# Kernel tuning notes

Hardware: AMD Instinct MI355X
Metric: run time of the kernel (lower is better)

## Reference

```python
import jax, jax.numpy as jnp
import numpy as np
from jax import lax

D_MODEL = 1024
D_INNER = 2048
B = 8
T = 2048
INIT_ALPHA_BIAS = 2.0


def setup_inputs() -> dict:
    key = jax.random.key(0)
    ks = jax.random.split(key, 6)
    def xavier(k, shape):
        fan_in, fan_out = shape[1], shape[0]
        lim = float(np.sqrt(6.0 / (fan_in + fan_out)))
        return jax.random.uniform(k, shape, jnp.float32, -lim, lim)
    return {
        "x": jax.random.normal(ks[0], (B, T, D_MODEL), jnp.float32),
        "h0": jnp.zeros((B, D_INNER), jnp.float32),
        "W_in": xavier(ks[1], (D_INNER, D_MODEL)),
        "W_alpha": xavier(ks[2], (D_INNER, D_INNER)),
        "b_alpha": jnp.full((D_INNER,), INIT_ALPHA_BIAS, jnp.float32),
        "W_v": xavier(ks[3], (D_INNER, D_INNER)),
        "b_v": jnp.zeros((D_INNER,), jnp.float32),
        "W_out": xavier(ks[4], (D_MODEL, D_INNER)),
    }


def reference(x, h0, W_in, W_alpha, b_alpha, W_v, b_v, W_out):
    # in_proj + silu pre-activation: [B,T,D_inner]
    x_proj = jax.nn.silu(jnp.einsum('btd,id->bti', x, W_in))
    # time-major for the scan: [T,B,D_inner]
    xr = jnp.transpose(x_proj, (1, 0, 2))
    # precompute gate and value for all steps (big GEMMs)
    alpha = jax.nn.sigmoid(jnp.einsum('tbd,ed->tbe', xr, W_alpha) + b_alpha)
    v = jnp.einsum('tbd,ed->tbe', xr, W_v) + b_v

    def step(h, av):
        a, vt = av
        h_new = a * h + (1.0 - a) * vt  # decay-gated update
        out_t = h_new * jax.nn.silu(h_new)  # self-gating
        return h_new, out_t

    h_final, outs = lax.scan(step, h0, (alpha, v))  # outs: [T,B,D_inner]
    # out_proj back to model dim, batch-major: [B,T,D_model]
    output = jnp.einsum('tbe,de->btd', outs, W_out)
    return output, h_final
```

## Files before the change

kernel.cpp:

```cpp
#include <hip/hip_runtime.h>
#include <cstdint>
#include <cstddef>

typedef unsigned short u16;
typedef unsigned int   u32;

#define D_MODEL 1024
#define D_INNER 2048
#define BATCH   8
#define TSEQ    2048
#define MROWS   (BATCH*TSEQ)
#define CHUNK   32
#define NCHUNK  (TSEQ/CHUNK)
#define EDIM    (BATCH*D_INNER)

typedef float  f32x4  __attribute__((ext_vector_type(4)));
typedef __bf16 bf16x8 __attribute__((ext_vector_type(8)));
typedef short  s16x8  __attribute__((ext_vector_type(8)));

__device__ __forceinline__ float bf2f(u16 u){ return __builtin_bit_cast(float, (u32)u << 16); }
__device__ __forceinline__ u16 f2bf(float f){
  u32 u = __builtin_bit_cast(u32, f);
  u += 0x7fffu + ((u >> 16) & 1u);
  return (u16)(u >> 16);
}
__device__ __forceinline__ float sigm(float x){ return 1.0f/(1.0f + __expf(-x)); }

__device__ __forceinline__ void gld16(const u16* g, u16* l){
  __builtin_amdgcn_global_load_lds((const __attribute__((address_space(1))) void*)g,
                                   (__attribute__((address_space(3))) void*)l, 16, 0, 0);
}

__device__ __forceinline__ s16x8 cvt8(const float* s){
  float4 u0 = *(const float4*)s;
  float4 u1 = *(const float4*)(s + 4);
  s16x8 p;
  p[0]=(short)f2bf(u0.x); p[1]=(short)f2bf(u0.y);
  p[2]=(short)f2bf(u0.z); p[3]=(short)f2bf(u0.w);
  p[4]=(short)f2bf(u1.x); p[5]=(short)f2bf(u1.y);
  p[6]=(short)f2bf(u1.z); p[7]=(short)f2bf(u1.w);
  return p;
}

template<int MODE, int K, int N>
__global__ __launch_bounds__(512, 2) void gemm256(
    const u16* __restrict__ A, const u16* __restrict__ Bt,
    const float* __restrict__ bias, void* __restrict__ Cout)
{
  __shared__ __align__(16) u16 sAB[2][2][16384];
  constexpr int NT = K/64;
  const int tid = threadIdx.x;
  const int w = tid >> 6, lane = tid & 63;
  const int wr = w >> 2, wc = w & 3;
  const int l15 = lane & 15, kg = lane >> 4;
  const int bm = blockIdx.x, bn = blockIdx.y;

  const int st_row8 = w*8 + (lane>>3);
  const int st_colb = ((lane&7)*16) ^ (((lane>>5)&1)<<5);
  const size_t a_base = (size_t)(bm*256) * K + (st_colb>>1);
  const size_t b_base = (size_t)(bn*256) * K + (st_colb>>1);

  auto stageA = [&](int buf, int kt, int upper){
    u16* dst = &sAB[0][buf][upper*8192 + w*512];
    #pragma unroll
    for (int i = 0; i < 2; ++i){
      int row = upper*128 + i*64 + st_row8;
      gld16(A + a_base + (size_t)row*K + kt*64, dst + i*4096);
    }
  };
  auto stageB = [&](int buf, int kt, int upper){
    u16* dst = &sAB[1][buf][upper*8192 + w*512];
    #pragma unroll
    for (int i = 0; i < 2; ++i){
      int row = upper*128 + i*64 + st_row8;
      gld16(Bt + b_base + (size_t)row*K + kt*64, dst + i*4096);
    }
  };

  const int sw   = ((l15>>2)&1)<<5;
  const int rdA0 = ((wr*128 + l15)*128 + kg*16) ^ sw;
  const int rdB0 = ((wc*64  + l15)*128 + kg*16) ^ sw;

  f32x4 acc[8][4] = {};

  stageA(0, 0, 0); stageB(0, 0, 0); stageA(0, 0, 1); stageB(0, 0, 1);
  asm volatile("s_waitcnt vmcnt(4)" ::: "memory");
  __builtin_amdgcn_s_barrier();

  for (int t = 0; t < NT; ++t){
    const char* As = (const char*)&sAB[0][t&1][0];
    const char* Bs = (const char*)&sAB[1][t&1][0];
    const int nb = (t+1)&1;
    const bool more = (t < NT-1);
    #pragma unroll
    for (int q = 0; q < 4; ++q){
      const int mh = (q>>1) ^ (q&1);
      const int nh = q>>1;
      s16x8 af[4][2], bf[2][2];
      #pragma unroll
      for (int mf = 0; mf < 4; ++mf)
        #pragma unroll
        for (int ks = 0; ks < 2; ++ks)
          af[mf][ks] = *(const s16x8*)(As + rdA0 + mh*8192 + mf*2048 + ks*64);
      #pragma unroll
      for (int nf = 0; nf < 2; ++nf)
        #pragma unroll
        for (int ks = 0; ks < 2; ++ks)
          bf[nf][ks] = *(const s16x8*)(Bs + rdB0 + nh*4096 + nf*2048 + ks*64);
      if (more){
        if      (q == 0) stageA(nb, t+1, 0);
        else if (q == 1) stageB(nb, t+1, 0);
        else if (q == 2) stageA(nb, t+1, 1);
        else             stageB(nb, t+1, 1);
        asm volatile("s_waitcnt vmcnt(4)" ::: "memory");
      } else {
        asm volatile("s_waitcnt vmcnt(0)" ::: "memory");
      }
      __builtin_amdgcn_s_barrier();
      __builtin_amdgcn_s_setprio(1);
      #pragma unroll
      for (int mf = 0; mf < 4; ++mf)
        #pragma unroll
        for (int nf = 0; nf < 2; ++nf)
          #pragma unroll
          for (int ks = 0; ks < 2; ++ks)
            acc[mh*4+mf][nh*2+nf] = __builtin_amdgcn_mfma_f32_16x16x32_bf16(
                __builtin_bit_cast(bf16x8, af[mf][ks]),
                __builtin_bit_cast(bf16x8, bf[nf][ks]),
                acc[mh*4+mf][nh*2+nf], 0, 0, 0);
      __builtin_amdgcn_s_setprio(0);
      __builtin_amdgcn_s_barrier();
    }
  }

  #pragma unroll
  for (int mi = 0; mi < 8; ++mi){
    #pragma unroll
    for (int ni = 0; ni < 4; ++ni){
      #pragma unroll
      for (int r = 0; r < 4; ++r){
        const int row = bm*256 + wr*128 + mi*16 + kg*4 + r;
        const int col = bn*256 + wc*64 + ni*16 + l15;
        float val = acc[mi][ni][r];
        if constexpr (MODE == 0){
          val = val * sigm(val);
          ((u16*)Cout)[(size_t)row*N + col] = f2bf(val);
        } else if constexpr (MODE == 1){
          val = sigm(val + bias[col]);
          ((u16*)Cout)[(size_t)row*N + col] = f2bf(val);
        } else if constexpr (MODE == 2){
          val = val + bias[col];
          ((u16*)Cout)[(size_t)row*N + col] = f2bf(val);
        } else {
          const int orow = (row & 7)*TSEQ + (row >> 3);
          ((float*)Cout)[(size_t)orow*N + col] = val;
        }
      }
    }
  }
}

template<int MODE, int K, int N, bool BA, bool BB>
__global__ __launch_bounds__(256) void gemm_bt(
    const void* __restrict__ Ap, const void* __restrict__ Bp,
    const float* __restrict__ bias, void* __restrict__ Cout)
{
  __shared__ __align__(16) u16 sA[128*32];
  __shared__ __align__(16) u16 sB[128*32];
  const int tid = threadIdx.x;
  const int bm = blockIdx.x, bn = blockIdx.y;
  const int w = tid >> 6, lane = tid & 63;
  const int wr = w >> 1, wc = w & 1;
  const int l15 = lane & 15, kg = lane >> 4;
  const int r0   = tid >> 2;
  const int koff = (tid & 3) * 8;

  int ga[2];
  #pragma unroll
  for (int i = 0; i < 2; ++i){
    int mc = bm*128 + r0 + i*64;
    if (MODE == 0)      ga[i] = (mc & 7) * TSEQ + (mc >> 3);
    else if (MODE == 3) ga[i] = (mc & (TSEQ-1)) * BATCH + (mc >> 11);
    else                ga[i] = mc;
  }
  const u16*   Abf = (const u16*)Ap;
  const float* Af  = (const float*)Ap;
  const u16*   Bbf = (const u16*)Bp;
  const float* Bf  = (const float*)Bp;
  u16* la[2] = { sA + w*512, sA + 2048 + w*512 };
  u16* lb[2] = { sB + w*512, sB + 2048 + w*512 };
  u16* ldsA = sA + tid*8;
  u16* ldsB = sB + tid*8;
  const int gb[2] = { bn*128 + r0, bn*128 + r0 + 64 };

  f32x4 acc[4][4] = {};
  for (int kt = 0; kt < K/32; ++kt){
    __syncthreads();
    if constexpr (BA){
      gld16(Abf + (size_t)ga[0]*K + koff + kt*32, la[0]);
      gld16(Abf + (size_t)ga[1]*K + koff + kt*32, la[1]);
    } else {
      #pragma unroll
      for (int i = 0; i < 2; ++i)
        *(s16x8*)(ldsA + i*2048) = cvt8(Af + (size_t)ga[i]*K + koff + kt*32);
    }
    if constexpr (BB){
      gld16(Bbf + (size_t)gb[0]*K + koff + kt*32, lb[0]);
      gld16(Bbf + (size_t)gb[1]*K + koff + kt*32, lb[1]);
    } else {
      #pragma unroll
      for (int i = 0; i < 2; ++i)
        *(s16x8*)(ldsB + i*2048) = cvt8(Bf + (size_t)gb[i]*K + koff + kt*32);
    }
    __syncthreads();

    s16x8 af[4], bfr[4];
    #pragma unroll
    for (int m = 0; m < 4; ++m)
      af[m] = *(const s16x8*)(sA + (wr*64 + m*16 + l15)*32 + kg*8);
    #pragma unroll
    for (int n = 0; n < 4; ++n)
      bfr[n] = *(const s16x8*)(sB + (wc*64 + n*16 + l15)*32 + kg*8);
    #pragma unroll
    for (int m = 0; m < 4; ++m)
      #pragma unroll
      for (int n = 0; n < 4; ++n)
        acc[m][n] = __builtin_amdgcn_mfma_f32_16x16x32_bf16(
            __builtin_bit_cast(bf16x8, af[m]),
            __builtin_bit_cast(bf16x8, bfr[n]),
            acc[m][n], 0, 0, 0);
  }
  #pragma unroll
  for (int m = 0; m < 4; ++m)
    #pragma unroll
    for (int n = 0; n < 4; ++n)
      #pragma unroll
      for (int r = 0; r < 4; ++r){
        const int row = bm*128 + wr*64 + m*16 + kg*4 + r;
        const int col = bn*128 + wc*64 + n*16 + l15;
        float val = acc[m][n][r];
        if constexpr (MODE == 0){
          val = val * sigm(val);
          ((u16*)Cout)[(size_t)row*N + col] = f2bf(val);
        } else if constexpr (MODE == 1){
          val = sigm(val + bias[col]);
          ((u16*)Cout)[(size_t)row*N + col] = f2bf(val);
        } else if constexpr (MODE == 2){
          val = val + bias[col];
          ((u16*)Cout)[(size_t)row*N + col] = f2bf(val);
        } else {
          ((float*)Cout)[(size_t)row*N + col] = val;
        }
      }
}

__global__ __launch_bounds__(256) void scan_pass1(
    const u16* __restrict__ alpha, const u16* __restrict__ v,
    float* __restrict__ P, float* __restrict__ H)
{
  const int e = blockIdx.x*256 + threadIdx.x;
  const int c = blockIdx.y;
  const size_t base = (size_t)c*CHUNK*EDIM + e;
  float p = 1.f, h = 0.f;
  #pragma unroll 8
  for (int t = 0; t < CHUNK; ++t){
    float a  = bf2f(alpha[base + (size_t)t*EDIM]);
    float vv = bf2f(v[base + (size_t)t*EDIM]);
    p *= a;
    h = a*h + (1.f - a)*vv;
  }
  P[(size_t)c*EDIM + e] = p;
  H[(size_t)c*EDIM + e] = h;
}

__global__ __launch_bounds__(256) void scan_pass2(
    const float* __restrict__ P, const float* __restrict__ H,
    const float* __restrict__ h0, float* __restrict__ hstart,
    float* __restrict__ hfinal)
{
  const int e = blockIdx.x*256 + threadIdx.x;
  float hs = h0[e];
  for (int c = 0; c < NCHUNK; ++c){
    hstart[(size_t)c*EDIM + e] = hs;
    hs = P[(size_t)c*EDIM + e]*hs + H[(size_t)c*EDIM + e];
  }
  hfinal[e] = hs;
}

__global__ __launch_bounds__(256) void scan_pass3(
    const u16* __restrict__ alpha, const u16* __restrict__ v,
    const float* __restrict__ hstart, u16* __restrict__ outs)
{
  const int e = blockIdx.x*256 + threadIdx.x;
  const int c = blockIdx.y;
  const size_t base = (size_t)c*CHUNK*EDIM + e;
  float h = hstart[(size_t)c*EDIM + e];
  #pragma unroll 8
  for (int t = 0; t < CHUNK; ++t){
    float a  = bf2f(alpha[base + (size_t)t*EDIM]);
    float vv = bf2f(v[base + (size_t)t*EDIM]);
    h = a*h + (1.f - a)*vv;
    float o = h*h*sigm(h);
    outs[base + (size_t)t*EDIM] = f2bf(o);
  }
}

__global__ __launch_bounds__(256) void cvt_bf16(
    const float* __restrict__ src, u16* __restrict__ dst, int n4)
{
  const int i = blockIdx.x*256 + threadIdx.x;
  if (i >= n4) return;
  const float4 f = ((const float4*)src)[i];
  u32 w0 = (u32)f2bf(f.x) | ((u32)f2bf(f.y) << 16);
  u32 w1 = (u32)f2bf(f.z) | ((u32)f2bf(f.w) << 16);
  ((uint2*)dst)[i] = make_uint2(w0, w1);
}

__global__ __launch_bounds__(256) void cvt_x_tm(
    const float* __restrict__ src, u16* __restrict__ dst)
{
  const int i = blockIdx.x*256 + threadIdx.x;
  const int d4  = i & 255;
  const int rin = i >> 8;
  const int b = rin >> 11, tt = rin & (TSEQ-1);
  const int rout = tt*BATCH + b;
  const float4 f = ((const float4*)src)[i];
  u32 w0 = (u32)f2bf(f.x) | ((u32)f2bf(f.y) << 16);
  u32 w1 = (u32)f2bf(f.z) | ((u32)f2bf(f.w) << 16);
  ((uint2*)dst)[(size_t)rout*256 + d4] = make_uint2(w0, w1);
}

extern "C" void kernel_launch(void* const* d_in, const int* in_sizes, int n_in,
                              void* d_out, int out_size, void* d_ws, size_t ws_size,
                              hipStream_t stream)
{
  const float* x     = (const float*)d_in[0];
  const float* h0    = (const float*)d_in[1];
  const float* W_in  = (const float*)d_in[2];
  const float* W_al  = (const float*)d_in[3];
  const float* b_al  = (const float*)d_in[4];
  const float* W_v   = (const float*)d_in[5];
  const float* b_v   = (const float*)d_in[6];
  const float* W_out = (const float*)d_in[7];

  float* out  = (float*)d_out;
  float* hfin = out + (size_t)MROWS*D_MODEL;

  const size_t SZ_ACT = (size_t)MROWS*D_INNER*2;
  const size_t SZ_ST  = (size_t)NCHUNK*EDIM*4;
  const size_t SZ_WI  = (size_t)D_INNER*D_MODEL*2;
  const size_t SZ_WA  = (size_t)D_INNER*D_INNER*2;
  const size_t need_min  = 3*SZ_ACT + 3*SZ_ST;
  const size_t need_fast = need_min + 2*SZ_WI + 2*SZ_WA + 8192;

  if (ws_size < need_min) return;

  char* ws = (char*)d_ws;
  auto carve = [&](size_t bytes){
    char* p = ws; ws += (bytes + 255) & ~(size_t)255; return p;
  };
  u16* xp   = (u16*)carve(SZ_ACT);
  u16* alp  = (u16*)carve(SZ_ACT);
  u16* vv   = (u16*)carve(SZ_ACT);
  float* P  = (float*)carve(SZ_ST);
  float* H  = (float*)carve(SZ_ST);
  float* hs = (float*)carve(SZ_ST);

  const dim3 gScan(EDIM/256, NCHUNK);

  auto cvt = [&](const float* s, u16* d, size_t n){
    int n4 = (int)(n/4);
    cvt_bf16<<<(n4+255)/256, 256, 0, stream>>>(s, d, n4);
  };

  if (ws_size >= need_fast){
    u16* wib = (u16*)carve(SZ_WI);
    u16* wab = (u16*)carve(SZ_WA);
    u16* wvb = (u16*)carve(SZ_WA);
    u16* wob = (u16*)carve(SZ_WI);
    u16* xb  = alp;

    cvt_x_tm<<<(MROWS*D_MODEL/4)/256, 256, 0, stream>>>(x, xb);
    cvt(W_in,  wib, (size_t)D_INNER*D_MODEL);
    cvt(W_al,  wab, (size_t)D_INNER*D_INNER);
    cvt(W_v,   wvb, (size_t)D_INNER*D_INNER);
    cvt(W_out, wob, (size_t)D_MODEL*D_INNER);

    gemm256<0, D_MODEL, D_INNER><<<dim3(MROWS/256, D_INNER/256), 512, 0, stream>>>(xb, wib, nullptr, xp);
    gemm256<1, D_INNER, D_INNER><<<dim3(MROWS/256, D_INNER/256), 512, 0, stream>>>(xp, wab, b_al,    alp);
    gemm256<2, D_INNER, D_INNER><<<dim3(MROWS/256, D_INNER/256), 512, 0, stream>>>(xp, wvb, b_v,     vv);

    scan_pass1<<<gScan, 256, 0, stream>>>(alp, vv, P, H);
    scan_pass2<<<EDIM/256, 256, 0, stream>>>(P, H, h0, hs, hfin);
    scan_pass3<<<gScan, 256, 0, stream>>>(alp, vv, hs, vv);

    gemm256<3, D_INNER, D_MODEL><<<dim3(MROWS/256, D_MODEL/256), 512, 0, stream>>>(vv, wob, nullptr, out);
  } else {
    const dim3 gBig(MROWS/128, D_INNER/128);
    const dim3 gOut(MROWS/128, D_MODEL/128);
    gemm_bt<0, D_MODEL, D_INNER, false, false><<<gBig, 256, 0, stream>>>(x,  W_in, nullptr, xp);
    gemm_bt<1, D_INNER, D_INNER, true,  false><<<gBig, 256, 0, stream>>>(xp, W_al, b_al,    alp);
    gemm_bt<2, D_INNER, D_INNER, true,  false><<<gBig, 256, 0, stream>>>(xp, W_v,  b_v,     vv);

    scan_pass1<<<gScan, 256, 0, stream>>>(alp, vv, P, H);
    scan_pass2<<<EDIM/256, 256, 0, stream>>>(P, H, h0, hs, hfin);
    scan_pass3<<<gScan, 256, 0, stream>>>(alp, vv, hs, vv);

    gemm_bt<3, D_INNER, D_MODEL, true, false><<<gOut, 256, 0, stream>>>(vv, W_out, nullptr, out);
  }
}
```

Before: 617.0 us.

## Fuse alpha and value GEMMs and restructure LDS swizzle and MFMA pipeline

Merges the gate and value projections into one GEMM with N doubled, writing sigmoid(gate) and biased value to two outputs by column range. This relies on the two bf16 weight buffers being contiguous in the workspace. Replaces the LDS XOR swizzle with a full 8-way row-based swizzle to cut bank conflicts. Reorders the main loop into four MFMA quadrants that reuse A and B fragments, staging next-tile A then B with a single wait. The fewer waits may expose more load latency.

```diff
diff --git a/kernel.cpp b/kernel.cpp
--- a/kernel.cpp
+++ b/kernel.cpp
@@ -42,10 +42,37 @@
   return p;
 }
 
+#define LOADA(AF, MH) \
+  _Pragma("unroll") \
+  for (int mf = 0; mf < 4; ++mf){ \
+    AF[mf][0] = *(const s16x8*)(As + (wr*128 + (MH)*64 + mf*16 + l15)*128 + csw); \
+    AF[mf][1] = *(const s16x8*)(As + (wr*128 + (MH)*64 + mf*16 + l15)*128 + (csw^64)); \
+  }
+#define LOADB(BF, NH) \
+  _Pragma("unroll") \
+  for (int nf = 0; nf < 2; ++nf){ \
+    BF[nf][0] = *(const s16x8*)(Bs + (wc*64 + (NH)*32 + nf*16 + l15)*128 + csw); \
+    BF[nf][1] = *(const s16x8*)(Bs + (wc*64 + (NH)*32 + nf*16 + l15)*128 + (csw^64)); \
+  }
+#define MFMAQ(AF, BF, MH, NH) \
+  __builtin_amdgcn_s_setprio(1); \
+  _Pragma("unroll") \
+  for (int mf = 0; mf < 4; ++mf) \
+    _Pragma("unroll") \
+    for (int nf = 0; nf < 2; ++nf) \
+      _Pragma("unroll") \
+      for (int ks = 0; ks < 2; ++ks) \
+        acc[(MH)*4+mf][(NH)*2+nf] = __builtin_amdgcn_mfma_f32_16x16x32_bf16( \
+            __builtin_bit_cast(bf16x8, AF[mf][ks]), \
+            __builtin_bit_cast(bf16x8, BF[nf][ks]), \
+            acc[(MH)*4+mf][(NH)*2+nf], 0, 0, 0); \
+  __builtin_amdgcn_s_setprio(0);
+
 template<int MODE, int K, int N>
 __global__ __launch_bounds__(512, 2) void gemm256(
     const u16* __restrict__ A, const u16* __restrict__ Bt,
-    const float* __restrict__ bias, void* __restrict__ Cout)
+    const float* __restrict__ bias, const float* __restrict__ bias2,
+    void* __restrict__ Cout, void* __restrict__ Cout2)
 {
   __shared__ __align__(16) u16 sAB[2][2][16384];
   constexpr int NT = K/64;
@@ -55,36 +82,30 @@
   const int l15 = lane & 15, kg = lane >> 4;
   const int bm = blockIdx.x, bn = blockIdx.y;
 
-  const int st_row8 = w*8 + (lane>>3);
-  const int st_colb = ((lane&7)*16) ^ (((lane>>5)&1)<<5);
-  const size_t a_base = (size_t)(bm*256) * K + (st_colb>>1);
-  const size_t b_base = (size_t)(bn*256) * K + (st_colb>>1);
+  const int st_row  = w*8 + (lane>>3);
+  const int st_cole = ((lane&7) ^ (lane>>3)) << 3;
+  const size_t a_base = (size_t)(bm*256)*K + st_cole;
+  const size_t b_base = (size_t)(bn*256)*K + st_cole;
 
   auto stageA = [&](int buf, int kt, int upper){
     u16* dst = &sAB[0][buf][upper*8192 + w*512];
     #pragma unroll
-    for (int i = 0; i < 2; ++i){
-      int row = upper*128 + i*64 + st_row8;
-      gld16(A + a_base + (size_t)row*K + kt*64, dst + i*4096);
-    }
+    for (int i = 0; i < 2; ++i)
+      gld16(A + a_base + (size_t)(upper*128 + i*64 + st_row)*K + kt*64, dst + i*4096);
   };
   auto stageB = [&](int buf, int kt, int upper){
     u16* dst = &sAB[1][buf][upper*8192 + w*512];
     #pragma unroll
-    for (int i = 0; i < 2; ++i){
-      int row = upper*128 + i*64 + st_row8;
-      gld16(Bt + b_base + (size_t)row*K + kt*64, dst + i*4096);
-    }
+    for (int i = 0; i < 2; ++i)
+      gld16(Bt + b_base + (size_t)(upper*128 + i*64 + st_row)*K + kt*64, dst + i*4096);
   };
 
-  const int sw   = ((l15>>2)&1)<<5;
-  const int rdA0 = ((wr*128 + l15)*128 + kg*16) ^ sw;
-  const int rdB0 = ((wc*64  + l15)*128 + kg*16) ^ sw;
+  const int csw = (kg*16) ^ ((l15&7)<<4);
 
   f32x4 acc[8][4] = {};
 
-  stageA(0, 0, 0); stageB(0, 0, 0); stageA(0, 0, 1); stageB(0, 0, 1);
-  asm volatile("s_waitcnt vmcnt(4)" ::: "memory");
+  stageA(0,0,0); stageB(0,0,0); stageA(0,0,1); stageB(0,0,1);
+  asm volatile("s_waitcnt vmcnt(0)" ::: "memory");
   __builtin_amdgcn_s_barrier();
 
   for (int t = 0; t < NT; ++t){
@@ -92,45 +113,30 @@
     const char* Bs = (const char*)&sAB[1][t&1][0];
     const int nb = (t+1)&1;
     const bool more = (t < NT-1);
-    #pragma unroll
-    for (int q = 0; q < 4; ++q){
-      const int mh = (q>>1) ^ (q&1);
-      const int nh = q>>1;
-      s16x8 af[4][2], bf[2][2];
-      #pragma unroll
-      for (int mf = 0; mf < 4; ++mf)
-        #pragma unroll
-        for (int ks = 0; ks < 2; ++ks)
-          af[mf][ks] = *(const s16x8*)(As + rdA0 + mh*8192 + mf*2048 + ks*64);
-      #pragma unroll
-      for (int nf = 0; nf < 2; ++nf)
-        #pragma unroll
-        for (int ks = 0; ks < 2; ++ks)
-          bf[nf][ks] = *(const s16x8*)(Bs + rdB0 + nh*4096 + nf*2048 + ks*64);
-      if (more){
-        if      (q == 0) stageA(nb, t+1, 0);
-        else if (q == 1) stageB(nb, t+1, 0);
-        else if (q == 2) stageA(nb, t+1, 1);
-        else             stageB(nb, t+1, 1);
-        asm volatile("s_waitcnt vmcnt(4)" ::: "memory");
-      } else {
-        asm volatile("s_waitcnt vmcnt(0)" ::: "memory");
-      }
-      __builtin_amdgcn_s_barrier();
-      __builtin_amdgcn_s_setprio(1);
-      #pragma unroll
-      for (int mf = 0; mf < 4; ++mf)
-        #pragma unroll
-        for (int nf = 0; nf < 2; ++nf)
-          #pragma unroll
-          for (int ks = 0; ks < 2; ++ks)
-            acc[mh*4+mf][nh*2+nf] = __builtin_amdgcn_mfma_f32_16x16x32_bf16(
-                __builtin_bit_cast(bf16x8, af[mf][ks]),
-                __builtin_bit_cast(bf16x8, bf[nf][ks]),
-                acc[mh*4+mf][nh*2+nf], 0, 0, 0);
-      __builtin_amdgcn_s_setprio(0);
-      __builtin_amdgcn_s_barrier();
-    }
+    s16x8 af[4][2], bf0[2][2], bf1[2][2];
+
+    LOADA(af, 0)
+    LOADB(bf0, 0)
+    if (more){ stageA(nb, t+1, 0); stageA(nb, t+1, 1); }
+    __builtin_amdgcn_s_barrier();
+    MFMAQ(af, bf0, 0, 0)
+    __builtin_amdgcn_s_barrier();
+
+    LOADB(bf1, 1)
+    if (more){ stageB(nb, t+1, 0); stageB(nb, t+1, 1); }
+    __builtin_amdgcn_s_barrier();
+    MFMAQ(af, bf1, 0, 1)
+    __builtin_amdgcn_s_barrier();
+
+    LOADA(af, 1)
+    __builtin_amdgcn_s_barrier();
+    MFMAQ(af, bf1, 1, 1)
+    __builtin_amdgcn_s_barrier();
+
+    asm volatile("s_waitcnt vmcnt(0)" ::: "memory");
+    __builtin_amdgcn_s_barrier();
+    MFMAQ(af, bf0, 1, 0)
+    __builtin_amdgcn_s_barrier();
   }
 
   #pragma unroll
@@ -145,15 +151,17 @@
         if constexpr (MODE == 0){
           val = val * sigm(val);
           ((u16*)Cout)[(size_t)row*N + col] = f2bf(val);
-        } else if constexpr (MODE == 1){
-          val = sigm(val + bias[col]);
-          ((u16*)Cout)[(size_t)row*N + col] = f2bf(val);
-        } else if constexpr (MODE == 2){
-          val = val + bias[col];
-          ((u16*)Cout)[(size_t)row*N + col] = f2bf(val);
-        } else {
+        } else if constexpr (MODE == 3){
           const int orow = (row & 7)*TSEQ + (row >> 3);
           ((float*)Cout)[(size_t)orow*N + col] = val;
+        } else if constexpr (MODE == 4){
+          if (col < D_INNER){
+            val = sigm(val + bias[col]);
+            ((u16*)Cout)[(size_t)row*D_INNER + col] = f2bf(val);
+          } else {
+            val = val + bias2[col - D_INNER];
+            ((u16*)Cout2)[(size_t)row*D_INNER + (col - D_INNER)] = f2bf(val);
+          }
         }
       }
     }
@@ -386,15 +394,17 @@
     cvt(W_v,   wvb, (size_t)D_INNER*D_INNER);
     cvt(W_out, wob, (size_t)D_MODEL*D_INNER);
 
-    gemm256<0, D_MODEL, D_INNER><<<dim3(MROWS/256, D_INNER/256), 512, 0, stream>>>(xb, wib, nullptr, xp);
-    gemm256<1, D_INNER, D_INNER><<<dim3(MROWS/256, D_INNER/256), 512, 0, stream>>>(xp, wab, b_al,    alp);
-    gemm256<2, D_INNER, D_INNER><<<dim3(MROWS/256, D_INNER/256), 512, 0, stream>>>(xp, wvb, b_v,     vv);
+    gemm256<0, D_MODEL, D_INNER><<<dim3(MROWS/256, D_INNER/256), 512, 0, stream>>>(
+        xb, wib, nullptr, nullptr, xp, nullptr);
+    gemm256<4, D_INNER, 2*D_INNER><<<dim3(MROWS/256, 2*D_INNER/256), 512, 0, stream>>>(
+        xp, wab, b_al, b_v, alp, vv);
 
     scan_pass1<<<gScan, 256, 0, stream>>>(alp, vv, P, H);
     scan_pass2<<<EDIM/256, 256, 0, stream>>>(P, H, h0, hs, hfin);
     scan_pass3<<<gScan, 256, 0, stream>>>(alp, vv, hs, vv);
 
-    gemm256<3, D_INNER, D_MODEL><<<dim3(MROWS/256, D_MODEL/256), 512, 0, stream>>>(vv, wob, nullptr, out);
+    gemm256<3, D_INNER, D_MODEL><<<dim3(MROWS/256, D_MODEL/256), 512, 0, stream>>>(
+        vv, wob, nullptr, nullptr, out, nullptr);
   } else {
     const dim3 gBig(MROWS/128, D_INNER/128);
     const dim3 gOut(MROWS/128, D_MODEL/128);
```

After: 547.5 us. -11.3%, faster.
